# Kernel tuning notes

Hardware: AMD Instinct MI355X
Metric: run time of the kernel (lower is better)

The kernel has to match this reference:

```python
import jax, jax.numpy as jnp
import numpy as np

N = 100000
E = 1600000
IN_DIM, HID, OUT = 256, 64, 32
NEG_SLOPE = 0.2
EPS = 1e-16


def setup_inputs() -> dict:
    key = jax.random.key(0)
    ks = jax.random.split(key, 10)
    s = lambda d: 1.0 / np.sqrt(d)
    return {
        "features": jax.random.normal(ks[0], (N, IN_DIM), dtype=jnp.float32),
        "edge_index": jax.random.randint(ks[1], (2, E), 0, N, dtype=jnp.int64),
        "w1": jax.random.normal(ks[2], (IN_DIM, HID), dtype=jnp.float32) * s(IN_DIM),
        "att_src": jax.random.normal(ks[3], (HID,), dtype=jnp.float32) * s(HID),
        "att_dst": jax.random.normal(ks[4], (HID,), dtype=jnp.float32) * s(HID),
        "w2": jax.random.normal(ks[5], (HID, OUT), dtype=jnp.float32) * s(HID),
        "l1_w": jax.random.normal(ks[6], (HID, OUT), dtype=jnp.float32) * s(OUT),
        "l1_b": jnp.zeros((HID,), dtype=jnp.float32),
        "l2_w": jax.random.normal(ks[7], (IN_DIM, HID), dtype=jnp.float32) * s(HID),
        "l2_b": jnp.zeros((IN_DIM,), dtype=jnp.float32),
    }


def gat_conv(x, W, a_src, a_dst, src, dst, n_nodes):
    # single-head GATConv, concat=False, no self loops, no bias
    h = x @ W                                   # [N, H]
    alpha_s = h @ a_src                         # [N]
    alpha_d = h @ a_dst                         # [N]
    e = alpha_s[src] + alpha_d[dst]             # [E]
    e = jnp.where(e > 0, e, NEG_SLOPE * e)      # LeakyReLU
    # segment softmax over incoming edges of each destination node
    m = jax.ops.segment_max(e, dst, num_segments=n_nodes)
    ex = jnp.exp(e - m[dst])
    z = jax.ops.segment_sum(ex, dst, num_segments=n_nodes)
    w = ex / (z[dst] + EPS)                     # [E]
    msg = w[:, None] * h[src]                   # [E, H]
    return jax.ops.segment_sum(msg, dst, num_segments=n_nodes)  # [N, H]


def reference(features, edge_index, w1, att_src, att_dst, w2, l1_w, l1_b, l2_w, l2_b):
    src, dst = edge_index[0], edge_index[1]
    h1 = jax.nn.elu(gat_conv(features, w1, att_src, att_dst, src, dst, N))
    h2 = h1 @ w2                                # conv2 with attention=False: plain linear
    h3 = jax.nn.elu(h2 @ l1_w.T + l1_b)
    h4 = h3 @ l2_w.T + l2_b
    return (h2, h4)
```

## Files before the change

kernel.cpp:

```cpp
#include <hip/hip_runtime.h>
#include <math.h>

constexpr int IN_DIM = 256;
constexpr int HID    = 64;
constexpr int OUTD   = 32;
#define NEG_SLOPE 0.2f
#define EPSV 1e-16f

__device__ __forceinline__ float eluf(float x) {
    return x > 0.f ? x : expm1f(x);
}

__device__ __forceinline__ unsigned short f32_to_bf16_rne(float f) {
    unsigned u = __float_as_uint(f);
    unsigned r = u + 0x7fffu + ((u >> 16) & 1u);
    return (unsigned short)(r >> 16);
}
__device__ __forceinline__ float bf16_bits_to_f32(unsigned short s) {
    return __uint_as_float(((unsigned)s) << 16);
}

__global__ void k_init(int* __restrict__ deg, int n) {
    int i = blockIdx.x * blockDim.x + threadIdx.x;
    int stride = gridDim.x * blockDim.x;
    for (; i < n; i += stride) deg[i] = 0;
}

__global__ __launch_bounds__(256) void k_wconv(
    const float* __restrict__ w2, const float* __restrict__ l1w,
    const float* __restrict__ l2w,
    short* __restrict__ w2f_hi, short* __restrict__ w2f_lo,
    short* __restrict__ l1f_hi, short* __restrict__ l1f_lo,
    short* __restrict__ l2f_hi, short* __restrict__ l2f_lo)
{
    int t = threadIdx.x;
    int lane = t & 63, combo = t >> 6;
    int lm = lane & 15, lg = lane >> 4;

    {
        int nt = combo >> 1, ks = combo & 1;
        #pragma unroll
        for (int i = 0; i < 8; ++i) {
            float f = w2[(size_t)(ks * 32 + lg * 8 + i) * 32 + nt * 16 + lm];
            unsigned short hb = f32_to_bf16_rne(f);
            float rem = f - bf16_bits_to_f32(hb);
            w2f_hi[((size_t)combo * 64 + lane) * 8 + i] = (short)hb;
            w2f_lo[((size_t)combo * 64 + lane) * 8 + i] = (short)f32_to_bf16_rne(rem);
        }
    }
    {
        int nt = combo;
        #pragma unroll
        for (int i = 0; i < 8; ++i) {
            float f = l1w[(size_t)(nt * 16 + lm) * 32 + lg * 8 + i];
            unsigned short hb = f32_to_bf16_rne(f);
            float rem = f - bf16_bits_to_f32(hb);
            l1f_hi[((size_t)combo * 64 + lane) * 8 + i] = (short)hb;
            l1f_lo[((size_t)combo * 64 + lane) * 8 + i] = (short)f32_to_bf16_rne(rem);
        }
    }
    for (int it = 0; it < 8; ++it) {
        int c = it * 4 + combo;
        int wv = c >> 3, ct = (c >> 1) & 3, ks = c & 1;
        #pragma unroll
        for (int i = 0; i < 8; ++i) {
            float f = l2w[(size_t)(wv * 64 + ct * 16 + lm) * 64 + ks * 32 + lg * 8 + i];
            unsigned short hb = f32_to_bf16_rne(f);
            float rem = f - bf16_bits_to_f32(hb);
            l2f_hi[((size_t)c * 64 + lane) * 8 + i] = (short)hb;
            l2f_lo[((size_t)c * 64 + lane) * 8 + i] = (short)f32_to_bf16_rne(rem);
        }
    }
}

__global__ __launch_bounds__(256) void k_feat_deg(
    const float* __restrict__ feat, const float* __restrict__ w1,
    const float* __restrict__ att_src, const float* __restrict__ att_dst,
    unsigned short* __restrict__ h_bf, float* __restrict__ as_,
    float* __restrict__ ad_,
    const int* __restrict__ ei, int* __restrict__ deg, int* __restrict__ rank,
    int n, int e, int nDegBlocks)
{
    typedef __attribute__((ext_vector_type(8))) short bx8;
    typedef __attribute__((ext_vector_type(4))) float fx4;

    __shared__ short a_hi[4 * 8 * 64 * 8];
    __shared__ short a_lo[4 * 8 * 64 * 8];
    __shared__ float al_part[2][4][64];

    int bid = blockIdx.x;
    int grp = bid / 5, pos = bid % 5;
    int t = threadIdx.x, lane = t & 63, wv = t >> 6;

    if (pos == 4) {
        if (grp >= nDegBlocks) return;
        int i = grp * 256 + t;
        int stride = nDegBlocks * 256;
        for (; i < e; i += stride) {
            int d = ei[(size_t)e + i];
            rank[i] = atomicAdd(&deg[d], 1);
        }
        return;
    }

    int fb = grp * 4 + pos;
    int base = fb * 64;
    if (base >= n) return;

    bx8 bhi[8], blo[8];
    {
        int nj = wv * 16 + (lane & 15);
        int kg = (lane >> 4) * 8;
        #pragma unroll
        for (int ks = 0; ks < 8; ++ks) {
            #pragma unroll
            for (int i = 0; i < 8; ++i) {
                float f = w1[(size_t)(ks * 32 + kg + i) * 64 + nj];
                unsigned short hb = f32_to_bf16_rne(f);
                float rem = f - bf16_bits_to_f32(hb);
                bhi[ks][i] = (short)hb;
                blo[ks][i] = (short)f32_to_bf16_rne(rem);
            }
        }
    }

    float4 v[16];
    #pragma unroll
    for (int c = 0; c < 8; ++c) {
        int node = (t >> 5) + c * 8;
        int oct = t & 31;
        int gn = base + node;
        if (gn < n) {
            const float4* fp = (const float4*)(feat + (size_t)gn * 256);
            v[2 * c]     = fp[oct * 2];
            v[2 * c + 1] = fp[oct * 2 + 1];
        } else {
            v[2 * c]     = make_float4(0.f, 0.f, 0.f, 0.f);
            v[2 * c + 1] = make_float4(0.f, 0.f, 0.f, 0.f);
        }
    }
    #pragma unroll
    for (int c = 0; c < 8; ++c) {
        int node = (t >> 5) + c * 8;
        int oct = t & 31;
        int mt = node >> 4, lm = node & 15;
        int ks = oct >> 2, lg = oct & 3;
        int flane = lg * 16 + lm;
        int idx = (((mt * 8 + ks) * 64) + (flane ^ ks)) * 8;
        float ff[8] = { v[2*c].x, v[2*c].y, v[2*c].z, v[2*c].w,
                        v[2*c+1].x, v[2*c+1].y, v[2*c+1].z, v[2*c+1].w };
        bx8 hv, lv;
        #pragma unroll
        for (int i = 0; i < 8; ++i) {
            unsigned short hb = f32_to_bf16_rne(ff[i]);
            float rem = ff[i] - bf16_bits_to_f32(hb);
            hv[i] = (short)hb;
            lv[i] = (short)f32_to_bf16_rne(rem);
        }
        *(bx8*)&a_hi[idx] = hv;
        *(bx8*)&a_lo[idx] = lv;
    }
    __syncthreads();

    fx4 acc[4];
    #pragma unroll
    for (int mt = 0; mt < 4; ++mt) acc[mt] = (fx4){0.f, 0.f, 0.f, 0.f};
    #pragma unroll
    for (int mt = 0; mt < 4; ++mt) {
        #pragma unroll
        for (int ks = 0; ks < 8; ++ks) {
            int idx = (((mt * 8 + ks) * 64) + (lane ^ ks)) * 8;
            bx8 ah = *(bx8*)&a_hi[idx];
            bx8 al = *(bx8*)&a_lo[idx];
            acc[mt] = __builtin_amdgcn_mfma_f32_16x16x32_bf16(ah, bhi[ks], acc[mt], 0, 0, 0);
            acc[mt] = __builtin_amdgcn_mfma_f32_16x16x32_bf16(ah, blo[ks], acc[mt], 0, 0, 0);
            acc[mt] = __builtin_amdgcn_mfma_f32_16x16x32_bf16(al, bhi[ks], acc[mt], 0, 0, 0);
        }
    }

    float asj = att_src[wv * 16 + (lane & 15)];
    float adj = att_dst[wv * 16 + (lane & 15)];
    #pragma unroll
    for (int mt = 0; mt < 4; ++mt) {
        #pragma unroll
        for (int r = 0; r < 4; ++r) {
            int lrow = mt * 16 + (lane >> 4) * 4 + r;
            int node = base + lrow;
            float hv = acc[mt][r];
            if (node < n)
                h_bf[(size_t)node * 64 + wv * 16 + (lane & 15)] = f32_to_bf16_rne(hv);
            float p1 = hv * asj, p2 = hv * adj;
            p1 += __shfl_xor(p1, 1);  p2 += __shfl_xor(p2, 1);
            p1 += __shfl_xor(p1, 2);  p2 += __shfl_xor(p2, 2);
            p1 += __shfl_xor(p1, 4);  p2 += __shfl_xor(p2, 4);
            p1 += __shfl_xor(p1, 8);  p2 += __shfl_xor(p2, 8);
            if ((lane & 15) == 0) {
                al_part[0][wv][lrow] = p1;
                al_part[1][wv][lrow] = p2;
            }
        }
    }
    __syncthreads();
    if (t < 64) {
        int node = base + t;
        if (node < n) {
            as_[node] = al_part[0][0][t] + al_part[0][1][t] + al_part[0][2][t] + al_part[0][3][t];
            ad_[node] = al_part[1][0][t] + al_part[1][1][t] + al_part[1][2][t] + al_part[1][3][t];
        }
    }
}

__global__ __launch_bounds__(1024) void k_scan_part(const int* __restrict__ deg,
                                                    int* __restrict__ part, int n) {
    __shared__ int wlds[16];
    int t = threadIdx.x, lane = t & 63, wv = t >> 6;
    int idx = blockIdx.x * 1024 + t;
    int v = (idx < n) ? deg[idx] : 0;
    #pragma unroll
    for (int s = 32; s > 0; s >>= 1) v += __shfl_xor(v, s);
    if (lane == 0) wlds[wv] = v;
    __syncthreads();
    if (t == 0) {
        int s = 0;
        #pragma unroll
        for (int w = 0; w < 16; ++w) s += wlds[w];
        part[blockIdx.x] = s;
    }
}

__global__ __launch_bounds__(1024) void k_scan_top(int* __restrict__ part,
                                                   int* __restrict__ off,
                                                   int nb, int n) {
    __shared__ int wsum[16];
    int t = threadIdx.x, lane = t & 63, wv = t >> 6;
    int v = (t < nb) ? part[t] : 0;
    int x = v;
    #pragma unroll
    for (int i = 1; i < 64; i <<= 1) {
        int u = __shfl_up(x, i);
        if (lane >= i) x += u;
    }
    if (lane == 63) wsum[wv] = x;
    __syncthreads();
    int add = 0;
    for (int w = 0; w < wv; ++w) add += wsum[w];
    if (t < nb) part[t] = x - v + add;
    if (t == nb - 1) off[n] = x + add;
}

__global__ __launch_bounds__(1024) void k_scan_down(const int* __restrict__ deg,
                                                    const int* __restrict__ part,
                                                    int* __restrict__ off, int n) {
    __shared__ int wsum[16];
    int t = threadIdx.x, lane = t & 63, wv = t >> 6;
    int idx = blockIdx.x * 1024 + t;
    int v = (idx < n) ? deg[idx] : 0;
    int x = v;
    #pragma unroll
    for (int i = 1; i < 64; i <<= 1) {
        int u = __shfl_up(x, i);
        if (lane >= i) x += u;
    }
    if (lane == 63) wsum[wv] = x;
    __syncthreads();
    int add = 0;
    for (int w = 0; w < wv; ++w) add += wsum[w];
    if (idx < n) off[idx] = x - v + add + part[blockIdx.x];
}

__global__ void k_fill(const int* __restrict__ ei, const float* __restrict__ as_,
                       const float* __restrict__ ad_, const int* __restrict__ off,
                       const int* __restrict__ rank, int2* __restrict__ edata,
                       int e, int lo, int hi) {
    int i = blockIdx.x * blockDim.x + threadIdx.x;
    int stride = gridDim.x * blockDim.x;
    for (; i < e; i += stride) {
        int d = ei[(size_t)e + i];
        if (d < lo || d >= hi) continue;
        int s = ei[i];
        float v = as_[s] + ad_[d];
        v = v > 0.f ? v : NEG_SLOPE * v;
        edata[off[d] + rank[i]] = make_int2(s, __float_as_int(v));
    }
}

__global__ __launch_bounds__(256) void k_gatw(const int* __restrict__ off,
                                              int2* __restrict__ edata, int n) {
    int lane = threadIdx.x & 63;
    int d = blockIdx.x * 4 + (threadIdx.x >> 6);
    if (d >= n) return;
    int beg = off[d], end = off[d + 1];
    float m = -3.0e38f;
    for (int i = beg + lane; i < end; i += 64)
        m = fmaxf(m, __int_as_float(edata[i].y));
    #pragma unroll
    for (int s = 32; s > 0; s >>= 1) m = fmaxf(m, __shfl_xor(m, s));

    int i0 = beg + lane;
    float e0 = 0.f, z = 0.f;
    if (i0 < end) { e0 = __expf(__int_as_float(edata[i0].y) - m); z = e0; }
    for (int i = i0 + 64; i < end; i += 64) {
        float e = __expf(__int_as_float(edata[i].y) - m);
        edata[i].y = __float_as_int(e);
        z += e;
    }
    #pragma unroll
    for (int s = 32; s > 0; s >>= 1) z += __shfl_xor(z, s);
    float rz = 1.f / (z + EPSV);
    if (i0 < end) edata[i0].y = __float_as_int(e0 * rz);
    for (int i = i0 + 64; i < end; i += 64)
        edata[i].y = __float_as_int(__int_as_float(edata[i].y) * rz);
}

__global__ __launch_bounds__(256) void k_gata(const int* __restrict__ off,
                                              const int2* __restrict__ edata,
                                              const unsigned short* __restrict__ h_bf,
                                              float* __restrict__ h1, int n) {
    int lane = threadIdx.x & 63;
    int d = blockIdx.x * 4 + (threadIdx.x >> 6);
    if (d >= n) return;
    int beg = off[d], end = off[d + 1];
    float a0 = 0.f, a1 = 0.f, a2 = 0.f, a3 = 0.f;
    int i = beg;
    for (; i + 4 <= end; i += 4) {
        int2 e0 = edata[i],     e1 = edata[i + 1];
        int2 e2 = edata[i + 2], e3 = edata[i + 3];
        float v0 = bf16_bits_to_f32(h_bf[(size_t)e0.x * 64 + lane]);
        float v1 = bf16_bits_to_f32(h_bf[(size_t)e1.x * 64 + lane]);
        float v2 = bf16_bits_to_f32(h_bf[(size_t)e2.x * 64 + lane]);
        float v3 = bf16_bits_to_f32(h_bf[(size_t)e3.x * 64 + lane]);
        a0 += __int_as_float(e0.y) * v0;
        a1 += __int_as_float(e1.y) * v1;
        a2 += __int_as_float(e2.y) * v2;
        a3 += __int_as_float(e3.y) * v3;
    }
    for (; i < end; ++i) {
        int2 ed = edata[i];
        a0 += __int_as_float(ed.y) * bf16_bits_to_f32(h_bf[(size_t)ed.x * 64 + lane]);
    }
    h1[(size_t)d * 64 + lane] = eluf((a0 + a1) + (a2 + a3));
}

__global__ __launch_bounds__(256) void k_mlp_fused(
    const float* __restrict__ h1g,
    const short* __restrict__ w2f_hi, const short* __restrict__ w2f_lo,
    const short* __restrict__ l1f_hi, const short* __restrict__ l1f_lo,
    const short* __restrict__ l2f_hi, const short* __restrict__ l2f_lo,
    const float* __restrict__ l1b, const float* __restrict__ l2b,
    float* __restrict__ oh2, float* __restrict__ oh4, int n)
{
    typedef __attribute__((ext_vector_type(8))) short bx8;
    typedef __attribute__((ext_vector_type(4))) float fx4;

    __shared__ float lds2[64 * 36];
    __shared__ float lds3[64 * 68];

    int t = threadIdx.x, lane = t & 63, wv = t >> 6;
    int base = blockIdx.x * 64;
    int lm = lane & 15, lg = lane >> 4;

    fx4 acc2[2];
    acc2[0] = (fx4){0.f, 0.f, 0.f, 0.f};
    acc2[1] = (fx4){0.f, 0.f, 0.f, 0.f};
    {
        bx8 ahi[2], alo[2];
        int row = base + wv * 16 + lm;
        const float* hp = h1g + (size_t)row * 64 + lg * 8;
        #pragma unroll
        for (int ks = 0; ks < 2; ++ks) {
            float4 a0, a1;
            if (row < n) {
                a0 = *(const float4*)(hp + ks * 32);
                a1 = *(const float4*)(hp + ks * 32 + 4);
            } else {
                a0 = make_float4(0.f, 0.f, 0.f, 0.f);
                a1 = make_float4(0.f, 0.f, 0.f, 0.f);
            }
            float ff[8] = { a0.x, a0.y, a0.z, a0.w, a1.x, a1.y, a1.z, a1.w };
            #pragma unroll
            for (int i = 0; i < 8; ++i) {
                unsigned short hb = f32_to_bf16_rne(ff[i]);
                float rem = ff[i] - bf16_bits_to_f32(hb);
                ahi[ks][i] = (short)hb;
                alo[ks][i] = (short)f32_to_bf16_rne(rem);
            }
        }
        #pragma unroll
        for (int nt = 0; nt < 2; ++nt) {
            #pragma unroll
            for (int ks = 0; ks < 2; ++ks) {
                int c = nt * 2 + ks;
                bx8 bh = *(const bx8*)&w2f_hi[((size_t)c * 64 + lane) * 8];
                bx8 bl = *(const bx8*)&w2f_lo[((size_t)c * 64 + lane) * 8];
                acc2[nt] = __builtin_amdgcn_mfma_f32_16x16x32_bf16(ahi[ks], bh, acc2[nt], 0, 0, 0);
                acc2[nt] = __builtin_amdgcn_mfma_f32_16x16x32_bf16(ahi[ks], bl, acc2[nt], 0, 0, 0);
                acc2[nt] = __builtin_amdgcn_mfma_f32_16x16x32_bf16(alo[ks], bh, acc2[nt], 0, 0, 0);
            }
        }
    }
    #pragma unroll
    for (int nt = 0; nt < 2; ++nt) {
        #pragma unroll
        for (int r = 0; r < 4; ++r) {
            int lrow = wv * 16 + lg * 4 + r;
            int node = base + lrow;
            float v = acc2[nt][r];
            if (node < n) oh2[(size_t)node * 32 + nt * 16 + lm] = v;
            lds2[lrow * 36 + nt * 16 + lm] = v;
        }
    }
    __syncthreads();

    fx4 acc3[4];
    #pragma unroll
    for (int nt = 0; nt < 4; ++nt) acc3[nt] = (fx4){0.f, 0.f, 0.f, 0.f};
    {
        bx8 ahi, alo;
        {
            const float* ap = &lds2[(wv * 16 + lm) * 36 + lg * 8];
            float4 a0 = *(const float4*)ap;
            float4 a1 = *(const float4*)(ap + 4);
            float ff[8] = { a0.x, a0.y, a0.z, a0.w, a1.x, a1.y, a1.z, a1.w };
            #pragma unroll
            for (int i = 0; i < 8; ++i) {
                unsigned short hb = f32_to_bf16_rne(ff[i]);
                float rem = ff[i] - bf16_bits_to_f32(hb);
                ahi[i] = (short)hb;
                alo[i] = (short)f32_to_bf16_rne(rem);
            }
        }
        #pragma unroll
        for (int nt = 0; nt < 4; ++nt) {
            bx8 bh = *(const bx8*)&l1f_hi[((size_t)nt * 64 + lane) * 8];
            bx8 bl = *(const bx8*)&l1f_lo[((size_t)nt * 64 + lane) * 8];
            acc3[nt] = __builtin_amdgcn_mfma_f32_16x16x32_bf16(ahi, bh, acc3[nt], 0, 0, 0);
            acc3[nt] = __builtin_amdgcn_mfma_f32_16x16x32_bf16(ahi, bl, acc3[nt], 0, 0, 0);
            acc3[nt] = __builtin_amdgcn_mfma_f32_16x16x32_bf16(alo, bh, acc3[nt], 0, 0, 0);
        }
    }
    #pragma unroll
    for (int nt = 0; nt < 4; ++nt) {
        float b = l1b[nt * 16 + lm];
        #pragma unroll
        for (int r = 0; r < 4; ++r) {
            int lrow = wv * 16 + lg * 4 + r;
            lds3[lrow * 68 + nt * 16 + lm] = eluf(acc3[nt][r] + b);
        }
    }
    __syncthreads();

    float bias[4];
    #pragma unroll
    for (int ct = 0; ct < 4; ++ct) bias[ct] = l2b[wv * 64 + ct * 16 + lm];

    #pragma unroll
    for (int mt = 0; mt < 4; ++mt) {
        bx8 ahi[2], alo[2];
        #pragma unroll
        for (int ks = 0; ks < 2; ++ks) {
            const float* ap = &lds3[(mt * 16 + lm) * 68 + ks * 32 + lg * 8];
            float4 a0 = *(const float4*)ap;
            float4 a1 = *(const float4*)(ap + 4);
            float ff[8] = { a0.x, a0.y, a0.z, a0.w, a1.x, a1.y, a1.z, a1.w };
            #pragma unroll
            for (int i = 0; i < 8; ++i) {
                unsigned short hb = f32_to_bf16_rne(ff[i]);
                float rem = ff[i] - bf16_bits_to_f32(hb);
                ahi[ks][i] = (short)hb;
                alo[ks][i] = (short)f32_to_bf16_rne(rem);
            }
        }
        fx4 acc[4];
        #pragma unroll
        for (int ct = 0; ct < 4; ++ct) acc[ct] = (fx4){0.f, 0.f, 0.f, 0.f};
        #pragma unroll
        for (int ct = 0; ct < 4; ++ct) {
            #pragma unroll
            for (int ks = 0; ks < 2; ++ks) {
                int c = wv * 8 + ct * 2 + ks;
                bx8 bh = *(const bx8*)&l2f_hi[((size_t)c * 64 + lane) * 8];
                bx8 bl = *(const bx8*)&l2f_lo[((size_t)c * 64 + lane) * 8];
                acc[ct] = __builtin_amdgcn_mfma_f32_16x16x32_bf16(ahi[ks], bh, acc[ct], 0, 0, 0);
                acc[ct] = __builtin_amdgcn_mfma_f32_16x16x32_bf16(ahi[ks], bl, acc[ct], 0, 0, 0);
                acc[ct] = __builtin_amdgcn_mfma_f32_16x16x32_bf16(alo[ks], bh, acc[ct], 0, 0, 0);
            }
        }
        #pragma unroll
        for (int ct = 0; ct < 4; ++ct) {
            #pragma unroll
            for (int r = 0; r < 4; ++r) {
                int orow = base + mt * 16 + lg * 4 + r;
                if (orow < n) {
                    int ocol = wv * 64 + ct * 16 + lm;
                    oh4[(size_t)orow * 256 + ocol] = acc[ct][r] + bias[ct];
                }
            }
        }
    }
}

extern "C" void kernel_launch(void* const* d_in, const int* in_sizes, int n_in,
                              void* d_out, int out_size, void* d_ws, size_t ws_size,
                              hipStream_t stream) {
    const float* feat    = (const float*)d_in[0];
    const int*   ei      = (const int*)d_in[1];
    const float* w1      = (const float*)d_in[2];
    const float* att_src = (const float*)d_in[3];
    const float* att_dst = (const float*)d_in[4];
    const float* w2      = (const float*)d_in[5];
    const float* l1w     = (const float*)d_in[6];
    const float* l1b     = (const float*)d_in[7];
    const float* l2w     = (const float*)d_in[8];
    const float* l2b     = (const float*)d_in[9];

    const int N = in_sizes[0] / IN_DIM;
    const int E = in_sizes[1] / 2;

    char* p = (char*)d_ws;
    auto alloc = [&](size_t bytes) {
        char* r = p;
        p += (bytes + 255) & ~(size_t)255;
        return r;
    };
    unsigned short* h_bf = (unsigned short*)alloc((size_t)N * HID * 2);
    float* h1g   = (float*)alloc((size_t)N * HID * 4);
    float* as_   = (float*)alloc((size_t)N * 4);
    float* ad_   = (float*)alloc((size_t)N * 4);
    int*   deg   = (int*)alloc((size_t)N * 4);
    int*   off   = (int*)alloc((size_t)(N + 1) * 4);
    int*   rank  = (int*)alloc((size_t)E * 4);
    int2*  edata = (int2*)alloc((size_t)E * 8);
    const int nb = (N + 1023) / 1024;
    int*   part  = (int*)alloc((size_t)nb * 4);
    short* w2f_hi = (short*)alloc(4 * 64 * 8 * 2);
    short* w2f_lo = (short*)alloc(4 * 64 * 8 * 2);
    short* l1f_hi = (short*)alloc(4 * 64 * 8 * 2);
    short* l1f_lo = (short*)alloc(4 * 64 * 8 * 2);
    short* l2f_hi = (short*)alloc(32 * 64 * 8 * 2);
    short* l2f_lo = (short*)alloc(32 * 64 * 8 * 2);

    float* oh2 = (float*)d_out;
    float* oh4 = oh2 + (size_t)N * OUTD;

    hipLaunchKernelGGL(k_init, dim3(256), dim3(256), 0, stream, deg, N);
    hipLaunchKernelGGL(k_wconv, dim3(1), dim3(256), 0, stream,
                       w2, l1w, l2w, w2f_hi, w2f_lo, l1f_hi, l1f_lo, l2f_hi, l2f_lo);
    const int nDegBlocks = 512;
    const int nFeatTiles = (N + 63) / 64;
    const int nGroups    = max((nFeatTiles + 3) / 4, nDegBlocks);
    hipLaunchKernelGGL(k_feat_deg, dim3(nGroups * 5), dim3(256), 0, stream,
                       feat, w1, att_src, att_dst, h_bf, as_, ad_,
                       ei, deg, rank, N, E, nDegBlocks);
    hipLaunchKernelGGL(k_scan_part, dim3(nb), dim3(1024), 0, stream, deg, part, N);
    hipLaunchKernelGGL(k_scan_top, dim3(1), dim3(1024), 0, stream, part, off, nb, N);
    hipLaunchKernelGGL(k_scan_down, dim3(nb), dim3(1024), 0, stream, deg, part, off, N);
    for (int pass = 0; pass < 4; ++pass) {
        int lo = (int)((size_t)N * pass / 4);
        int hi = (int)((size_t)N * (pass + 1) / 4);
        hipLaunchKernelGGL(k_fill, dim3(2048), dim3(256), 0, stream,
                           ei, as_, ad_, off, rank, edata, E, lo, hi);
    }
    hipLaunchKernelGGL(k_gatw, dim3((N + 3) / 4), dim3(256), 0, stream, off, edata, N);
    hipLaunchKernelGGL(k_gata, dim3((N + 3) / 4), dim3(256), 0, stream,
                       off, edata, h_bf, h1g, N);
    hipLaunchKernelGGL(k_mlp_fused, dim3((N + 63) / 64), dim3(256), 0, stream,
                       h1g, w2f_hi, w2f_lo, l1f_hi, l1f_lo, l2f_hi, l2f_lo,
                       l1b, l2b, oh2, oh4, N);
}
```

Before: 273.0 us.

## Fuse GAT softmax and aggregation, recompute logits, store h1 as bf16

Merges the separate softmax-weight and aggregation kernels into one kernel that recomputes edge logits from per-node attention scalars rather than storing them. The CSR edge array shrinks from int2 to int source indices, and weights are broadcast across the wavefront with shuffles. It also stores h1 as bf16 and drops the lo-part MFMA correction in the first MLP matmul, so h1 loses precision. The aim is to cut global memory traffic in edge fill, softmax and MLP input; the cost is three gathers of as_ per edge and lower accuracy in h2/h4.

```diff
diff --git a/kernel.cpp b/kernel.cpp
--- a/kernel.cpp
+++ b/kernel.cpp
@@ -268,81 +268,82 @@
     if (idx < n) off[idx] = x - v + add + part[blockIdx.x];
 }
 
-__global__ void k_fill(const int* __restrict__ ei, const float* __restrict__ as_,
-                       const float* __restrict__ ad_, const int* __restrict__ off,
-                       const int* __restrict__ rank, int2* __restrict__ edata,
+__global__ void k_fill(const int* __restrict__ ei, const int* __restrict__ off,
+                       const int* __restrict__ rank, int* __restrict__ srcs,
                        int e, int lo, int hi) {
     int i = blockIdx.x * blockDim.x + threadIdx.x;
     int stride = gridDim.x * blockDim.x;
     for (; i < e; i += stride) {
         int d = ei[(size_t)e + i];
         if (d < lo || d >= hi) continue;
-        int s = ei[i];
-        float v = as_[s] + ad_[d];
-        v = v > 0.f ? v : NEG_SLOPE * v;
-        edata[off[d] + rank[i]] = make_int2(s, __float_as_int(v));
-    }
-}
-
-__global__ __launch_bounds__(256) void k_gatw(const int* __restrict__ off,
-                                              int2* __restrict__ edata, int n) {
+        srcs[off[d] + rank[i]] = ei[i];
+    }
+}
+
+__global__ __launch_bounds__(256) void k_gat(const int* __restrict__ off,
+                                             const int* __restrict__ srcs,
+                                             const float* __restrict__ as_,
+                                             const float* __restrict__ ad_,
+                                             const unsigned short* __restrict__ h_bf,
+                                             unsigned short* __restrict__ h1b, int n) {
     int lane = threadIdx.x & 63;
     int d = blockIdx.x * 4 + (threadIdx.x >> 6);
     if (d >= n) return;
     int beg = off[d], end = off[d + 1];
+    float adv = ad_[d];
+
     float m = -3.0e38f;
-    for (int i = beg + lane; i < end; i += 64)
-        m = fmaxf(m, __int_as_float(edata[i].y));
+    for (int i = beg + lane; i < end; i += 64) {
+        float ev = as_[srcs[i]] + adv;
+        ev = ev > 0.f ? ev : NEG_SLOPE * ev;
+        m = fmaxf(m, ev);
+    }
     #pragma unroll
     for (int s = 32; s > 0; s >>= 1) m = fmaxf(m, __shfl_xor(m, s));
 
-    int i0 = beg + lane;
-    float e0 = 0.f, z = 0.f;
-    if (i0 < end) { e0 = __expf(__int_as_float(edata[i0].y) - m); z = e0; }
-    for (int i = i0 + 64; i < end; i += 64) {
-        float e = __expf(__int_as_float(edata[i].y) - m);
-        edata[i].y = __float_as_int(e);
-        z += e;
+    float z = 0.f;
+    for (int i = beg + lane; i < end; i += 64) {
+        float ev = as_[srcs[i]] + adv;
+        ev = ev > 0.f ? ev : NEG_SLOPE * ev;
+        z += __expf(ev - m);
     }
     #pragma unroll
     for (int s = 32; s > 0; s >>= 1) z += __shfl_xor(z, s);
     float rz = 1.f / (z + EPSV);
-    if (i0 < end) edata[i0].y = __float_as_int(e0 * rz);
-    for (int i = i0 + 64; i < end; i += 64)
-        edata[i].y = __float_as_int(__int_as_float(edata[i].y) * rz);
-}
-
-__global__ __launch_bounds__(256) void k_gata(const int* __restrict__ off,
-                                              const int2* __restrict__ edata,
-                                              const unsigned short* __restrict__ h_bf,
-                                              float* __restrict__ h1, int n) {
-    int lane = threadIdx.x & 63;
-    int d = blockIdx.x * 4 + (threadIdx.x >> 6);
-    if (d >= n) return;
-    int beg = off[d], end = off[d + 1];
+
     float a0 = 0.f, a1 = 0.f, a2 = 0.f, a3 = 0.f;
-    int i = beg;
-    for (; i + 4 <= end; i += 4) {
-        int2 e0 = edata[i],     e1 = edata[i + 1];
-        int2 e2 = edata[i + 2], e3 = edata[i + 3];
-        float v0 = bf16_bits_to_f32(h_bf[(size_t)e0.x * 64 + lane]);
-        float v1 = bf16_bits_to_f32(h_bf[(size_t)e1.x * 64 + lane]);
-        float v2 = bf16_bits_to_f32(h_bf[(size_t)e2.x * 64 + lane]);
-        float v3 = bf16_bits_to_f32(h_bf[(size_t)e3.x * 64 + lane]);
-        a0 += __int_as_float(e0.y) * v0;
-        a1 += __int_as_float(e1.y) * v1;
-        a2 += __int_as_float(e2.y) * v2;
-        a3 += __int_as_float(e3.y) * v3;
-    }
-    for (; i < end; ++i) {
-        int2 ed = edata[i];
-        a0 += __int_as_float(ed.y) * bf16_bits_to_f32(h_bf[(size_t)ed.x * 64 + lane]);
-    }
-    h1[(size_t)d * 64 + lane] = eluf((a0 + a1) + (a2 + a3));
+    for (int chunk = beg; chunk < end; chunk += 64) {
+        int idx = chunk + lane;
+        int sreg = 0; float wreg = 0.f;
+        if (idx < end) {
+            sreg = srcs[idx];
+            float ev = as_[sreg] + adv;
+            ev = ev > 0.f ? ev : NEG_SLOPE * ev;
+            wreg = __expf(ev - m) * rz;
+        }
+        int cnt = min(64, end - chunk);
+        int j = 0;
+        for (; j + 4 <= cnt; j += 4) {
+            int   s0 = __shfl(sreg, j),     s1 = __shfl(sreg, j + 1);
+            int   s2 = __shfl(sreg, j + 2), s3 = __shfl(sreg, j + 3);
+            float w0 = __shfl(wreg, j),     w1 = __shfl(wreg, j + 1);
+            float w2 = __shfl(wreg, j + 2), w3 = __shfl(wreg, j + 3);
+            a0 += w0 * bf16_bits_to_f32(h_bf[(size_t)s0 * 64 + lane]);
+            a1 += w1 * bf16_bits_to_f32(h_bf[(size_t)s1 * 64 + lane]);
+            a2 += w2 * bf16_bits_to_f32(h_bf[(size_t)s2 * 64 + lane]);
+            a3 += w3 * bf16_bits_to_f32(h_bf[(size_t)s3 * 64 + lane]);
+        }
+        for (; j < cnt; ++j) {
+            int   sj = __shfl(sreg, j);
+            float wj = __shfl(wreg, j);
+            a0 += wj * bf16_bits_to_f32(h_bf[(size_t)sj * 64 + lane]);
+        }
+    }
+    h1b[(size_t)d * 64 + lane] = f32_to_bf16_rne(eluf((a0 + a1) + (a2 + a3)));
 }
 
 __global__ __launch_bounds__(256) void k_mlp_fused(
-    const float* __restrict__ h1g,
+    const unsigned short* __restrict__ h1b,
     const short* __restrict__ w2f_hi, const short* __restrict__ w2f_lo,
     const short* __restrict__ l1f_hi, const short* __restrict__ l1f_lo,
     const short* __restrict__ l2f_hi, const short* __restrict__ l2f_lo,
@@ -363,27 +364,14 @@
     acc2[0] = (fx4){0.f, 0.f, 0.f, 0.f};
     acc2[1] = (fx4){0.f, 0.f, 0.f, 0.f};
     {
-        bx8 ahi[2], alo[2];
+        bx8 ahi[2];
         int row = base + wv * 16 + lm;
-        const float* hp = h1g + (size_t)row * 64 + lg * 8;
         #pragma unroll
         for (int ks = 0; ks < 2; ++ks) {
-            float4 a0, a1;
-            if (row < n) {
-                a0 = *(const float4*)(hp + ks * 32);
-                a1 = *(const float4*)(hp + ks * 32 + 4);
-            } else {
-                a0 = make_float4(0.f, 0.f, 0.f, 0.f);
-                a1 = make_float4(0.f, 0.f, 0.f, 0.f);
-            }
-            float ff[8] = { a0.x, a0.y, a0.z, a0.w, a1.x, a1.y, a1.z, a1.w };
-            #pragma unroll
-            for (int i = 0; i < 8; ++i) {
-                unsigned short hb = f32_to_bf16_rne(ff[i]);
-                float rem = ff[i] - bf16_bits_to_f32(hb);
-                ahi[ks][i] = (short)hb;
-                alo[ks][i] = (short)f32_to_bf16_rne(rem);
-            }
+            if (row < n)
+                ahi[ks] = *(const bx8*)(h1b + (size_t)row * 64 + ks * 32 + lg * 8);
+            else
+                ahi[ks] = (bx8){0, 0, 0, 0, 0, 0, 0, 0};
         }
         #pragma unroll
         for (int nt = 0; nt < 2; ++nt) {
@@ -394,7 +382,6 @@
                 bx8 bl = *(const bx8*)&w2f_lo[((size_t)c * 64 + lane) * 8];
                 acc2[nt] = __builtin_amdgcn_mfma_f32_16x16x32_bf16(ahi[ks], bh, acc2[nt], 0, 0, 0);
                 acc2[nt] = __builtin_amdgcn_mfma_f32_16x16x32_bf16(ahi[ks], bl, acc2[nt], 0, 0, 0);
-                acc2[nt] = __builtin_amdgcn_mfma_f32_16x16x32_bf16(alo[ks], bh, acc2[nt], 0, 0, 0);
             }
         }
     }
@@ -523,13 +510,13 @@
         return r;
     };
     unsigned short* h_bf = (unsigned short*)alloc((size_t)N * HID * 2);
-    float* h1g   = (float*)alloc((size_t)N * HID * 4);
+    unsigned short* h1b  = (unsigned short*)alloc((size_t)N * HID * 2);
     float* as_   = (float*)alloc((size_t)N * 4);
     float* ad_   = (float*)alloc((size_t)N * 4);
     int*   deg   = (int*)alloc((size_t)N * 4);
     int*   off   = (int*)alloc((size_t)(N + 1) * 4);
     int*   rank  = (int*)alloc((size_t)E * 4);
-    int2*  edata = (int2*)alloc((size_t)E * 8);
+    int*   srcs  = (int*)alloc((size_t)E * 4);
     const int nb = (N + 1023) / 1024;
     int*   part  = (int*)alloc((size_t)nb * 4);
     short* w2f_hi = (short*)alloc(4 * 64 * 8 * 2);
@@ -558,12 +545,11 @@
         int lo = (int)((size_t)N * pass / 4);
         int hi = (int)((size_t)N * (pass + 1) / 4);
         hipLaunchKernelGGL(k_fill, dim3(2048), dim3(256), 0, stream,
-                           ei, as_, ad_, off, rank, edata, E, lo, hi);
-    }
-    hipLaunchKernelGGL(k_gatw, dim3((N + 3) / 4), dim3(256), 0, stream, off, edata, N);
-    hipLaunchKernelGGL(k_gata, dim3((N + 3) / 4), dim3(256), 0, stream,
-                       off, edata, h_bf, h1g, N);
+                           ei, off, rank, srcs, E, lo, hi);
+    }
+    hipLaunchKernelGGL(k_gat, dim3((N + 3) / 4), dim3(256), 0, stream,
+                       off, srcs, as_, ad_, h_bf, h1b, N);
     hipLaunchKernelGGL(k_mlp_fused, dim3((N + 63) / 64), dim3(256), 0, stream,
-                       h1g, w2f_hi, w2f_lo, l1f_hi, l1f_lo, l2f_hi, l2f_lo,
+                       h1b, w2f_hi, w2f_lo, l1f_hi, l1f_lo, l2f_hi, l2f_lo,
                        l1b, l2b, oh2, oh4, N);
 }
```

Measured after the change: 240.6 us. 1.13x faster.
